# Optimization experiments

Measured on AMD Instinct MI355X. Metric: run time of the kernel, lower is better.

## Reference

```python
import jax, jax.numpy as jnp
import numpy as np

BATCH, SEQ, E, H = 8, 2048, 1024, 1024
LEAK = 0.95
SPECTRAL_RADIUS = 1.2
SPARSITY = 0.1


def setup_inputs() -> dict:
    rng = np.random.default_rng(0)
    x = rng.standard_normal((BATCH, SEQ, E)).astype(np.float32)
    # W_in: kaiming_uniform-like init
    bound = np.sqrt(1.0 / E)
    W_in = rng.uniform(-bound, bound, (H, E)).astype(np.float32)
    # W_res: sparse normal, rescaled to spectral radius 1.2
    W_res = rng.standard_normal((H, H)).astype(np.float32)
    mask = (rng.random((H, H)) > SPARSITY).astype(np.float32)
    W_res *= mask
    rad = np.max(np.abs(np.linalg.eigvals(W_res.astype(np.float64))))
    W_res = (W_res * (SPECTRAL_RADIUS / (rad + 1e-8))).astype(np.float32)
    s = 0.02
    inp = {
        "x": jnp.asarray(x),
        "W_in": jnp.asarray(W_in),
        "W_res": jnp.asarray(W_res),
        "norm_g": jnp.ones((E,), jnp.float32),
        "norm_b": jnp.zeros((E,), jnp.float32),
        "delta_w": jnp.asarray(rng.standard_normal((1, E)).astype(np.float32) * s),
        "delta_b": jnp.zeros((1,), jnp.float32),
        "A": jnp.full((H,), -10.0, jnp.float32),
        "B_w": jnp.asarray(rng.standard_normal((H, E)).astype(np.float32) * s),
        "ro_g": jnp.ones((H,), jnp.float32),
        "ro_b": jnp.zeros((H,), jnp.float32),
        "ro_w": jnp.asarray(rng.standard_normal((E, H)).astype(np.float32) * s),
        "ro_bias": jnp.zeros((E,), jnp.float32),
        "gate_w": jnp.asarray(rng.standard_normal((E, E)).astype(np.float32) * s),
        "gate_b": jnp.zeros((E,), jnp.float32),
    }
    return inp


def _layernorm(x, g, b, eps=1e-5):
    m = jnp.mean(x, axis=-1, keepdims=True)
    v = jnp.mean((x - m) ** 2, axis=-1, keepdims=True)
    return (x - m) * jax.lax.rsqrt(v + eps) * g + b


def reference(x, W_in, W_res, norm_g, norm_b, delta_w, delta_b, A, B_w,
              ro_g, ro_b, ro_w, ro_bias, gate_w, gate_b):
    x_norm = _layernorm(x, norm_g, norm_b)                      # [B,S,E]

    # --- TrueReservoir: leaky tanh RNN (scan over seq) ---
    xin = jnp.einsum('bse,he->bsh', x_norm, W_in)               # [B,S,H]
    h0 = jnp.zeros((x.shape[0], W_res.shape[0]), x.dtype)

    def res_step(h, u):
        new = jnp.tanh(u + h @ W_res.T)
        new = LEAK * new + (1.0 - LEAK) * h
        return new, new

    _, res_states = jax.lax.scan(res_step, h0, jnp.swapaxes(xin, 0, 1))
    res_states = jnp.swapaxes(res_states, 0, 1)                 # [B,S,H]

    ro_in = _layernorm(res_states, ro_g, ro_b)
    reservoir_out = jax.nn.gelu(jnp.einsum('bsh,eh->bse', ro_in, ro_w) + ro_bias,
                                approximate=False)              # [B,S,E]

    # --- selective SSM-style scan ---
    Bx = jnp.einsum('bse,he->bsh', x_norm, B_w)                 # [B,S,H]
    delta = jax.nn.softplus(jnp.einsum('bse,oe->bso', x_norm, delta_w) + delta_b)  # [B,S,1]
    A_bar = jnp.exp(A * delta)                                  # [B,S,H]
    B_bar = Bx * (1.0 - A_bar) / (A + 1e-8)                     # [B,S,H]

    def ssm_step(h, ab):
        a, b = ab
        h = a * h + b
        return h, h

    _, ssm_states = jax.lax.scan(
        ssm_step, h0, (jnp.swapaxes(A_bar, 0, 1), jnp.swapaxes(B_bar, 0, 1)))
    ssm_states = jnp.swapaxes(ssm_states, 0, 1)                 # [B,S,H]

    gate = jax.nn.sigmoid(jnp.einsum('bse,fe->bsf', x, gate_w) + gate_b)  # [B,S,E]
    return reservoir_out * gate + ssm_states * (1.0 - gate)
```

## Files before the change

kernel.cpp:

```cpp
#include <hip/hip_runtime.h>
#include <math.h>

#define B_ 8
#define S_ 2048
#define E_ 1024
#define H_ 1024
#define M_ 16384

typedef __attribute__((ext_vector_type(8))) short short8;
typedef __attribute__((ext_vector_type(4))) float floatx4;

__device__ __forceinline__ void block_reduce2(float &a, float &b) {
#pragma unroll
  for (int off = 32; off > 0; off >>= 1) {
    a += __shfl_down(a, off);
    b += __shfl_down(b, off);
  }
  __shared__ float sa[4], sb[4];
  const int w = threadIdx.x >> 6;
  __syncthreads();
  if ((threadIdx.x & 63) == 0) { sa[w] = a; sb[w] = b; }
  __syncthreads();
  a = sa[0] + sa[1] + sa[2] + sa[3];
  b = sb[0] + sb[1] + sb[2] + sb[3];
}

__device__ __forceinline__ unsigned pack_bf16(float lo, float hi) {
  return __builtin_amdgcn_perm(__float_as_uint(hi) + 0x8000u,
                               __float_as_uint(lo) + 0x8000u, 0x07060302u);
}
__device__ __forceinline__ unsigned pack_hi16(unsigned a, unsigned b) {
  return __builtin_amdgcn_perm(b, a, 0x07060302u);
}

__global__ __launch_bounds__(256) void ln_delta_kernel(
    const float* __restrict__ x, const float* __restrict__ g, const float* __restrict__ bt,
    const float* __restrict__ dw, const float* __restrict__ db,
    unsigned short* __restrict__ xnb, float* __restrict__ delta)
{
  const int row = blockIdx.x;
  const int t = threadIdx.x;
  const float4 v = ((const float4*)(x + (size_t)row * E_))[t];
  float s1 = v.x + v.y + v.z + v.w;
  float s2 = v.x*v.x + v.y*v.y + v.z*v.z + v.w*v.w;
  block_reduce2(s1, s2);
  const float mean = s1 * (1.f / E_);
  const float var  = s2 * (1.f / E_) - mean * mean;
  const float rstd = rsqrtf(var + 1e-5f);
  const float4 g4 = ((const float4*)g)[t];
  const float4 b4 = ((const float4*)bt)[t];
  float4 o;
  o.x = (v.x - mean) * rstd * g4.x + b4.x;
  o.y = (v.y - mean) * rstd * g4.y + b4.y;
  o.z = (v.z - mean) * rstd * g4.z + b4.z;
  o.w = (v.w - mean) * rstd * g4.w + b4.w;
  uint2 p;
  p.x = pack_bf16(o.x, o.y); p.y = pack_bf16(o.z, o.w);
  ((uint2*)(xnb + (size_t)row * E_))[t] = p;
  const float4 d4 = ((const float4*)dw)[t];
  float dd = o.x*d4.x + o.y*d4.y + o.z*d4.z + o.w*d4.w;
  float dummy = 0.f;
  block_reduce2(dd, dummy);
  if (t == 0) {
    const float z = dd + db[0];
    delta[row] = (z > 20.f) ? z : log1pf(__expf(z));
  }
}

__global__ __launch_bounds__(256) void rowstats_kernel(
    const float* __restrict__ res, float2* __restrict__ st)
{
  const int row = blockIdx.x;
  const int t = threadIdx.x;
  const float4 v = ((const float4*)(res + (size_t)row * H_))[t];
  float s1 = v.x + v.y + v.z + v.w;
  float s2 = v.x*v.x + v.y*v.y + v.z*v.z + v.w*v.w;
  block_reduce2(s1, s2);
  if (t == 0) {
    const float m = s1 * (1.f / H_);
    const float var = s2 * (1.f / H_) - m * m;
    st[row] = make_float2(m, rsqrtf(var + 1e-5f));
  }
}

__global__ __launch_bounds__(256) void tobf16_kernel(
    const float* __restrict__ s, unsigned short* __restrict__ d)
{
  const int i = blockIdx.x * 256 + threadIdx.x;
  const float4 v = ((const float4*)s)[i];
  uint2 p;
  p.x = pack_bf16(v.x, v.y); p.y = pack_bf16(v.z, v.w);
  ((uint2*)d)[i] = p;
}

__global__ __launch_bounds__(256) void splitw_kernel(
    const float* __restrict__ s, unsigned short* __restrict__ dh, unsigned short* __restrict__ dl)
{
  const int i = blockIdx.x * 256 + threadIdx.x;
  const float4 v = ((const float4*)s)[i];
  const float sv[4] = {v.x, v.y, v.z, v.w};
  unsigned h[4]; float l[4];
#pragma unroll
  for (int e = 0; e < 4; ++e) {
    h[e] = (__float_as_uint(sv[e]) + 0x8000u) & 0xFFFF0000u;
    l[e] = sv[e] - __uint_as_float(h[e]);
  }
  uint2 ph, pl;
  ph.x = pack_hi16(h[0], h[1]); ph.y = pack_hi16(h[2], h[3]);
  pl.x = pack_bf16(l[0], l[1]); pl.y = pack_bf16(l[2], l[3]);
  ((uint2*)dh)[i] = ph;
  ((uint2*)dl)[i] = pl;
}

__global__ __launch_bounds__(256) void gemm_bb(
    const unsigned short* __restrict__ A, const unsigned short* __restrict__ W,
    float* __restrict__ C)
{
  __shared__ __align__(16) unsigned short As[128 * 40];
  __shared__ __align__(16) unsigned short Ws[128 * 40];
  const int tid  = threadIdx.x;
  const int bn   = blockIdx.x & 7;
  const int bm   = blockIdx.x >> 3;
  const int wave = tid >> 6, lane = tid & 63;
  const int wm = (wave >> 1) * 64, wn = (wave & 1) * 64;
  const int fm = lane & 15, quad = lane >> 4;

  floatx4 acc[4][4];
#pragma unroll
  for (int i = 0; i < 4; ++i)
#pragma unroll
    for (int j = 0; j < 4; ++j) acc[i][j] = (floatx4){0.f, 0.f, 0.f, 0.f};

  const unsigned short* Abase = A + (size_t)bm * 128 * 1024;
  const unsigned short* Wbase = W + (size_t)bn * 128 * 1024;

  for (int k0 = 0; k0 < 1024; k0 += 32) {
    uint2 a2[4], w2[4];
#pragma unroll
    for (int i = 0; i < 4; ++i) {
      const int q = tid + 256 * i;
      const int row = q >> 3, ch = q & 7;
      a2[i] = *(const uint2*)(Abase + (size_t)row * 1024 + k0 + ch * 4);
      w2[i] = *(const uint2*)(Wbase + (size_t)row * 1024 + k0 + ch * 4);
    }
#pragma unroll
    for (int i = 0; i < 4; ++i) {
      const int q = tid + 256 * i;
      const int row = q >> 3, ch = q & 7;
      *(uint2*)(&As[row * 40 + ch * 4]) = a2[i];
      *(uint2*)(&Ws[row * 40 + ch * 4]) = w2[i];
    }
    __syncthreads();
    short8 af[4], wf[4];
#pragma unroll
    for (int i = 0; i < 4; ++i) {
      af[i] = *(const short8*)(&As[(wm + i * 16 + fm) * 40 + quad * 8]);
      wf[i] = *(const short8*)(&Ws[(wn + i * 16 + fm) * 40 + quad * 8]);
    }
#pragma unroll
    for (int i = 0; i < 4; ++i)
#pragma unroll
      for (int j = 0; j < 4; ++j)
        acc[i][j] = __builtin_amdgcn_mfma_f32_16x16x32_bf16(af[i], wf[j], acc[i][j], 0, 0, 0);
    __syncthreads();
  }

#pragma unroll
  for (int i = 0; i < 4; ++i) {
    const int grow0 = bm * 128 + wm + i * 16 + quad * 4;
#pragma unroll
    for (int j = 0; j < 4; ++j) {
      const int gcol = bn * 128 + wn + j * 16 + fm;
#pragma unroll
      for (int r = 0; r < 4; ++r)
        C[(size_t)(grow0 + r) * 1024 + gcol] = acc[i][j][r];
    }
  }
}

template<int ACT>
__global__ __launch_bounds__(256) void gemm_bf16_nt(
    const float* __restrict__ A, const float* __restrict__ W,
    const float* __restrict__ bias, float* __restrict__ C)
{
  __shared__ __align__(16) unsigned short As[128 * 40];
  __shared__ __align__(16) unsigned short Ws[128 * 40];
  const int tid  = threadIdx.x;
  const int bn   = blockIdx.x & 7;
  const int bm   = blockIdx.x >> 3;
  const int wave = tid >> 6, lane = tid & 63;
  const int wm = (wave >> 1) * 64, wn = (wave & 1) * 64;
  const int fm = lane & 15, quad = lane >> 4;

  floatx4 acc[4][4];
#pragma unroll
  for (int i = 0; i < 4; ++i)
#pragma unroll
    for (int j = 0; j < 4; ++j) acc[i][j] = (floatx4){0.f, 0.f, 0.f, 0.f};

  const float* Abase = A + (size_t)bm * 128 * 1024;
  const float* Wbase = W + (size_t)bn * 128 * 1024;

  for (int k0 = 0; k0 < 1024; k0 += 32) {
    float4 a4[4], w4[4];
#pragma unroll
    for (int i = 0; i < 4; ++i) {
      const int q = tid + 256 * i;
      const int row = q >> 3, ch = q & 7;
      a4[i] = *(const float4*)(Abase + (size_t)row * 1024 + k0 + ch * 4);
      w4[i] = *(const float4*)(Wbase + (size_t)row * 1024 + k0 + ch * 4);
    }
#pragma unroll
    for (int i = 0; i < 4; ++i) {
      const int q = tid + 256 * i;
      const int row = q >> 3, ch = q & 7;
      uint2 pa, pw;
      pa.x = pack_bf16(a4[i].x, a4[i].y); pa.y = pack_bf16(a4[i].z, a4[i].w);
      pw.x = pack_bf16(w4[i].x, w4[i].y); pw.y = pack_bf16(w4[i].z, w4[i].w);
      *(uint2*)(&As[row * 40 + ch * 4]) = pa;
      *(uint2*)(&Ws[row * 40 + ch * 4]) = pw;
    }
    __syncthreads();
    short8 af[4], wf[4];
#pragma unroll
    for (int i = 0; i < 4; ++i) {
      af[i] = *(const short8*)(&As[(wm + i * 16 + fm) * 40 + quad * 8]);
      wf[i] = *(const short8*)(&Ws[(wn + i * 16 + fm) * 40 + quad * 8]);
    }
#pragma unroll
    for (int i = 0; i < 4; ++i)
#pragma unroll
      for (int j = 0; j < 4; ++j)
        acc[i][j] = __builtin_amdgcn_mfma_f32_16x16x32_bf16(af[i], wf[j], acc[i][j], 0, 0, 0);
    __syncthreads();
  }

#pragma unroll
  for (int i = 0; i < 4; ++i) {
    const int grow0 = bm * 128 + wm + i * 16 + quad * 4;
#pragma unroll
    for (int j = 0; j < 4; ++j) {
      const int gcol = bn * 128 + wn + j * 16 + fm;
      const float bb = (ACT == 1) ? bias[gcol] : 0.f;
#pragma unroll
      for (int r = 0; r < 4; ++r) {
        float v = acc[i][j][r] + bb;
        if (ACT == 1) v = 1.f / (1.f + __expf(-v));
        C[(size_t)(grow0 + r) * 1024 + gcol] = v;
      }
    }
  }
}

__global__ __launch_bounds__(256) void gemm_readout_mfma(
    const float* __restrict__ A,
    const unsigned short* __restrict__ Wh_g,
    const unsigned short* __restrict__ Wl_g,
    const float* __restrict__ bias,
    const float2* __restrict__ lnst,
    const float* __restrict__ lng, const float* __restrict__ lnb,
    const float* __restrict__ Avec,
    const float* __restrict__ cumd,
    const float* __restrict__ chH,
    const float* __restrict__ gate,
    float* __restrict__ C)
{
  __shared__ __align__(16) unsigned short Ah[128 * 40];
  __shared__ __align__(16) unsigned short Al[128 * 40];
  __shared__ __align__(16) unsigned short Wh[128 * 40];
  __shared__ __align__(16) unsigned short Wl[128 * 40];
  const int tid  = threadIdx.x;
  const int bn   = blockIdx.x & 7;
  const int bm   = blockIdx.x >> 3;
  const int wave = tid >> 6, lane = tid & 63;
  const int wm = (wave >> 1) * 64, wn = (wave & 1) * 64;
  const int fm = lane & 15, quad = lane >> 4;

  floatx4 acc[4][4];
#pragma unroll
  for (int i = 0; i < 4; ++i)
#pragma unroll
    for (int j = 0; j < 4; ++j) acc[i][j] = (floatx4){0.f, 0.f, 0.f, 0.f};

  const float* Abase = A + (size_t)bm * 128 * 1024;
  const unsigned short* Whb = Wh_g + (size_t)bn * 128 * 1024;
  const unsigned short* Wlb = Wl_g + (size_t)bn * 128 * 1024;

  float2 st_i[4];
#pragma unroll
  for (int i = 0; i < 4; ++i) {
    const int q = tid + 256 * i;
    st_i[i] = lnst[bm * 128 + (q >> 3)];
  }

  for (int k0 = 0; k0 < 1024; k0 += 32) {
#pragma unroll
    for (int i = 0; i < 4; ++i) {
      const int q = tid + 256 * i;
      const int row = q >> 3, ch = q & 7;
      float4 a4 = *(const float4*)(Abase + (size_t)row * 1024 + k0 + ch * 4);
      const float4 g4 = *(const float4*)(lng + k0 + ch * 4);
      const float4 b4 = *(const float4*)(lnb + k0 + ch * 4);
      const float2 st = st_i[i];
      a4.x = (a4.x - st.x) * st.y * g4.x + b4.x;
      a4.y = (a4.y - st.x) * st.y * g4.y + b4.y;
      a4.z = (a4.z - st.x) * st.y * g4.z + b4.z;
      a4.w = (a4.w - st.x) * st.y * g4.w + b4.w;
      const float av[4] = {a4.x, a4.y, a4.z, a4.w};
      unsigned ah[4]; float alr[4];
#pragma unroll
      for (int e = 0; e < 4; ++e) {
        ah[e] = (__float_as_uint(av[e]) + 0x8000u) & 0xFFFF0000u;
        alr[e] = av[e] - __uint_as_float(ah[e]);
      }
      uint2 pah, pal;
      pah.x = pack_hi16(ah[0], ah[1]); pah.y = pack_hi16(ah[2], ah[3]);
      pal.x = pack_bf16(alr[0], alr[1]); pal.y = pack_bf16(alr[2], alr[3]);
      *(uint2*)(&Ah[row * 40 + ch * 4]) = pah;
      *(uint2*)(&Al[row * 40 + ch * 4]) = pal;
      *(uint2*)(&Wh[row * 40 + ch * 4]) = *(const uint2*)(Whb + (size_t)row * 1024 + k0 + ch * 4);
      *(uint2*)(&Wl[row * 40 + ch * 4]) = *(const uint2*)(Wlb + (size_t)row * 1024 + k0 + ch * 4);
    }
    __syncthreads();
    short8 afh[4], afl[4], wfh[4], wfl[4];
#pragma unroll
    for (int i = 0; i < 4; ++i) {
      const int ao = (wm + i * 16 + fm) * 40 + quad * 8;
      const int wo = (wn + i * 16 + fm) * 40 + quad * 8;
      afh[i] = *(const short8*)(&Ah[ao]);
      afl[i] = *(const short8*)(&Al[ao]);
      wfh[i] = *(const short8*)(&Wh[wo]);
      wfl[i] = *(const short8*)(&Wl[wo]);
    }
#pragma unroll
    for (int i = 0; i < 4; ++i)
#pragma unroll
      for (int j = 0; j < 4; ++j) {
        acc[i][j] = __builtin_amdgcn_mfma_f32_16x16x32_bf16(afh[i], wfh[j], acc[i][j], 0, 0, 0);
        acc[i][j] = __builtin_amdgcn_mfma_f32_16x16x32_bf16(afl[i], wfh[j], acc[i][j], 0, 0, 0);
        acc[i][j] = __builtin_amdgcn_mfma_f32_16x16x32_bf16(afh[i], wfl[j], acc[i][j], 0, 0, 0);
      }
    __syncthreads();
  }

#pragma unroll
  for (int i = 0; i < 4; ++i) {
    const int grow0 = bm * 128 + wm + i * 16 + quad * 4;
    float cd_r[4];
    int hb_r[4];
#pragma unroll
    for (int r = 0; r < 4; ++r) {
      const int gr = grow0 + r;
      const int b = gr >> 11;
      const int c = (gr & 2047) >> 7;
      cd_r[r] = cumd[gr];
      hb_r[r] = (b * 16 + c) << 10;
    }
#pragma unroll
    for (int j = 0; j < 4; ++j) {
      const int gcol = bn * 128 + wn + j * 16 + fm;
      const float Ae = Avec[gcol];
      const float bb = bias[gcol];
#pragma unroll
      for (int r = 0; r < 4; ++r) {
        const int gr = grow0 + r;
        const size_t off = (size_t)gr * 1024 + gcol;
        const float hin = chH[hb_r[r] + gcol];
        const float lcl = C[off];
        const float gt  = gate[off];
        float v = acc[i][j][r] + bb;
        v = 0.5f * v * (1.f + erff(v * 0.70710678118654752f));
        const float p = __expf(Ae * cd_r[r]);
        const float sst = lcl + p * hin;
        C[off] = v * gt + sst * (1.f - gt);
      }
    }
  }
}

__global__ __launch_bounds__(512, 2) void reservoir_scan_kernel(
    float* __restrict__ xin_res,
    const float* __restrict__ Wres,
    unsigned* __restrict__ hbuf,
    unsigned* __restrict__ unused)
{
  const int tid = threadIdx.x;
  const int wg  = blockIdx.x;
  const int go  = wg >> 4;
  const int mem = wg & 15;
  const int g   = tid >> 6;
  const int l   = tid & 63;
  const int row8 = mem * 64 + g * 8;

  __shared__ __align__(16) float hs[2][1024];

  float4 w4[8][4];
  {
#pragma unroll
    for (int r = 0; r < 8; ++r) {
      const float* wrow = Wres + (size_t)(row8 + r) * 1024 + l * 16;
#pragma unroll
      for (int j = 0; j < 4; ++j) w4[r][j] = *(const float4*)(wrow + 4 * j);
    }
  }

  const int m0 = l & 1, m1 = (l >> 1) & 1, m2 = (l >> 2) & 1;
  const int myrow = row8 + (l & 7);
  float hprev = 0.f;
  const unsigned long long tmask = 0x0000FFFF0000FFFFull;

  const int Pw = (tid >> 1) ^ ((tid >> 6) & 7);
  const int wofs = Pw * 4 + (tid & 1) * 2;

  for (int s = 0; s < S_; ++s) {
    const float u = xin_res[((size_t)go * S_ + s) * H_ + myrow];
    asm volatile("" :: "v"(u));

    const unsigned tag = (unsigned)s & 0xFFFFu;
    const unsigned long long tag2 = (unsigned long long)tag | ((unsigned long long)tag << 32);
    const unsigned long long* hp =
        (const unsigned long long*)(hbuf + (size_t)(s & 1) * 8192 + go * 1024) + tid;
    unsigned long long w;
    for (;;) {
      w = __hip_atomic_load(hp, __ATOMIC_RELAXED, __HIP_MEMORY_SCOPE_AGENT);
      if (((w ^ tag2) & tmask) == 0ull) break;
    }

    float2 hf;
    hf.x = __uint_as_float((unsigned)w & 0xFFFF0000u);
    hf.y = __uint_as_float((unsigned)(w >> 32) & 0xFFFF0000u);
    *(float2*)(&hs[s & 1][wofs]) = hf;
    __syncthreads();

    const float* hbse = hs[s & 1];
    float acc0 = 0.f, acc1 = 0.f, acc2 = 0.f, acc3 = 0.f;
    float acc4 = 0.f, acc5 = 0.f, acc6 = 0.f, acc7 = 0.f;
#pragma unroll
    for (int j = 0; j < 4; ++j) {
      const int P = (4 * l + j) ^ ((l >> 3) & 7);
      const float4 h4 = *(const float4*)(hbse + P * 4);
      acc0 += w4[0][j].x * h4.x + w4[0][j].y * h4.y + w4[0][j].z * h4.z + w4[0][j].w * h4.w;
      acc1 += w4[1][j].x * h4.x + w4[1][j].y * h4.y + w4[1][j].z * h4.z + w4[1][j].w * h4.w;
      acc2 += w4[2][j].x * h4.x + w4[2][j].y * h4.y + w4[2][j].z * h4.z + w4[2][j].w * h4.w;
      acc3 += w4[3][j].x * h4.x + w4[3][j].y * h4.y + w4[3][j].z * h4.z + w4[3][j].w * h4.w;
      acc4 += w4[4][j].x * h4.x + w4[4][j].y * h4.y + w4[4][j].z * h4.z + w4[4][j].w * h4.w;
      acc5 += w4[5][j].x * h4.x + w4[5][j].y * h4.y + w4[5][j].z * h4.z + w4[5][j].w * h4.w;
      acc6 += w4[6][j].x * h4.x + w4[6][j].y * h4.y + w4[6][j].z * h4.z + w4[6][j].w * h4.w;
      acc7 += w4[7][j].x * h4.x + w4[7][j].y * h4.y + w4[7][j].z * h4.z + w4[7][j].w * h4.w;
    }

    float v0 = (m0 ? acc1 : acc0) + __shfl_xor(m0 ? acc0 : acc1, 1);
    float v1 = (m0 ? acc3 : acc2) + __shfl_xor(m0 ? acc2 : acc3, 1);
    float v2 = (m0 ? acc5 : acc4) + __shfl_xor(m0 ? acc4 : acc5, 1);
    float v3 = (m0 ? acc7 : acc6) + __shfl_xor(m0 ? acc6 : acc7, 1);
    float u0 = (m1 ? v1 : v0) + __shfl_xor(m1 ? v0 : v1, 2);
    float u1 = (m1 ? v3 : v2) + __shfl_xor(m1 ? v2 : v3, 2);
    float ps = (m2 ? u1 : u0) + __shfl_xor(m2 ? u0 : u1, 4);
    ps += __shfl_xor(ps, 8);
    ps += __shfl_xor(ps, 16);
    ps += __shfl_xor(ps, 32);

    const float z  = u + ps;
    const float e  = __expf(2.f * z);
    const float hn = 1.f - __fdividef(2.f, e + 1.f);
    const float hv = 0.95f * hn + 0.05f * hprev;
    hprev = hv;

    if (l < 8) {
      const unsigned word = ((__float_as_uint(hv) + 0x8000u) & 0xFFFF0000u)
                          | ((unsigned)(s + 1) & 0xFFFFu);
      __hip_atomic_store(hbuf + (size_t)((s + 1) & 1) * 8192 + go * 1024 + myrow, word,
                         __ATOMIC_RELAXED, __HIP_MEMORY_SCOPE_AGENT);
      xin_res[((size_t)go * S_ + s) * H_ + myrow] = hv;
    }
  }
}

__global__ __launch_bounds__(128) void cumd_kernel(
    const float* __restrict__ delta, float* __restrict__ cumd)
{
  const int t = threadIdx.x;
  const int b = t >> 4, c = t & 15;
  const int base = b * S_ + c * 128;
  float acc = 0.f;
  for (int i = 0; i < 128; ++i) { acc += delta[base + i]; cumd[base + i] = acc; }
}

__global__ __launch_bounds__(256) void ssm_partial_kernel(
    const float* __restrict__ delta, const float* __restrict__ Avec,
    float* __restrict__ bx, float* __restrict__ P)
{
  const int idx = blockIdx.x * 256 + threadIdx.x;
  const int h = idx & 1023;
  const int c = (idx >> 10) & 15;
  const int b = idx >> 14;
  const float Ah = Avec[h];
  const float inv = 1.f / (Ah + 1e-8f);
  const float* dp = delta + b * S_ + c * 128;
  float* xp = bx + ((size_t)(b * S_ + c * 128)) * H_ + h;
  float p = 1.f, hl = 0.f;
  for (int t = 0; t < 128; ++t) {
    const float a = __expf(Ah * dp[t]);
    const float bb = xp[(size_t)t * H_] * (1.f - a) * inv;
    hl = a * hl + bb;
    p *= a;
    xp[(size_t)t * H_] = hl;
  }
  P[(b * 16 + c) * 1024 + h] = p;
}

__global__ __launch_bounds__(256) void ssm_combine_kernel(
    const float* __restrict__ P, const float* __restrict__ local, float* __restrict__ Hin)
{
  const int idx = blockIdx.x * 256 + threadIdx.x;
  const int h = idx & 1023;
  const int b = idx >> 10;
  float hh = 0.f;
#pragma unroll
  for (int c = 0; c < 16; ++c) {
    const int o = (b * 16 + c) * 1024 + h;
    Hin[o] = hh;
    hh = P[o] * hh + local[((size_t)(b * S_ + c * 128 + 127)) * H_ + h];
  }
}

extern "C" void kernel_launch(void* const* d_in, const int* in_sizes, int n_in,
                              void* d_out, int out_size, void* d_ws, size_t ws_size,
                              hipStream_t stream) {
  (void)in_sizes; (void)n_in; (void)out_size; (void)ws_size;
  const float* x      = (const float*)d_in[0];
  const float* W_in   = (const float*)d_in[1];
  const float* W_res  = (const float*)d_in[2];
  const float* norm_g = (const float*)d_in[3];
  const float* norm_b = (const float*)d_in[4];
  const float* dw     = (const float*)d_in[5];
  const float* db     = (const float*)d_in[6];
  const float* Avec   = (const float*)d_in[7];
  const float* B_w    = (const float*)d_in[8];
  const float* ro_g   = (const float*)d_in[9];
  const float* ro_b   = (const float*)d_in[10];
  const float* ro_w   = (const float*)d_in[11];
  const float* ro_bias= (const float*)d_in[12];
  const float* gate_w = (const float*)d_in[13];
  const float* gate_b = (const float*)d_in[14];
  float* out = (float*)d_out;
  float* ws  = (float*)d_ws;

  float*    buf0   = ws;
  float*    buf1   = ws + 16777216;
  float*    delta  = ws + 33554432;
  float*    cumd   = ws + 33570816;
  unsigned* hbuf   = (unsigned*)(ws + 33587200);
  float2*   stats  = (float2*)(ws + 33603712);
  float*    chP    = ws + 33636480;
  float*    chH    = ws + 33767552;
  unsigned short* xnb = (unsigned short*)buf0;
  unsigned short* wib = (unsigned short*)(ws + 33898624);
  unsigned short* bwb = (unsigned short*)(ws + 34422912);
  unsigned short* roh = (unsigned short*)(ws + 34947200);
  unsigned short* rol = (unsigned short*)(ws + 35471488);

  tobf16_kernel<<<1024, 256, 0, stream>>>(W_in, wib);
  tobf16_kernel<<<1024, 256, 0, stream>>>(B_w, bwb);
  splitw_kernel<<<1024, 256, 0, stream>>>(ro_w, roh, rol);
  ln_delta_kernel<<<M_, 256, 0, stream>>>(x, norm_g, norm_b, dw, db, xnb, delta);
  gemm_bb<<<1024, 256, 0, stream>>>(xnb, wib, buf1);
  gemm_bb<<<1024, 256, 0, stream>>>(xnb, bwb, out);
  gemm_bf16_nt<1><<<1024, 256, 0, stream>>>(x, gate_w, gate_b, buf0);
  cumd_kernel<<<1, 128, 0, stream>>>(delta, cumd);
  ssm_partial_kernel<<<512, 256, 0, stream>>>(delta, Avec, out, chP);
  ssm_combine_kernel<<<32, 256, 0, stream>>>(chP, out, chH);
  hipMemsetAsync(hbuf, 0, 2 * 8192 * sizeof(unsigned), stream);
  reservoir_scan_kernel<<<128, 512, 0, stream>>>(buf1, W_res, hbuf, nullptr);
  rowstats_kernel<<<M_, 256, 0, stream>>>(buf1, stats);
  gemm_readout_mfma<<<1024, 256, 0, stream>>>(buf1, roh, rol, ro_bias, stats, ro_g, ro_b,
                                              Avec, cumd, chH, buf0, out);
}
```

Before: 3.989 ms.

## Fuse gate GEMM into reservoir scan launch to overlap on idle CUs

The sigmoid gate GEMM no longer runs as its own kernel. It is folded into the reservoir scan launch as 1024 extra workgroups (block index 128 and up), so the GEMM can fill compute units the 128 latency-bound scan workgroups leave idle. The GEMM blocks use 512 threads but only 256 are active, and shared memory is reused through a common byte buffer. A risk is that GEMM blocks compete with the spin-waiting scan blocks for CU resources and memory bandwidth. The cross-workgroup flag protocol also assumes all 128 scan blocks stay co-resident, which ordering by block index makes likely.

```diff
diff --git a/kernel.cpp b/kernel.cpp
--- a/kernel.cpp
+++ b/kernel.cpp
@@ -178,80 +178,6 @@
   }
 }
 
-template<int ACT>
-__global__ __launch_bounds__(256) void gemm_bf16_nt(
-    const float* __restrict__ A, const float* __restrict__ W,
-    const float* __restrict__ bias, float* __restrict__ C)
-{
-  __shared__ __align__(16) unsigned short As[128 * 40];
-  __shared__ __align__(16) unsigned short Ws[128 * 40];
-  const int tid  = threadIdx.x;
-  const int bn   = blockIdx.x & 7;
-  const int bm   = blockIdx.x >> 3;
-  const int wave = tid >> 6, lane = tid & 63;
-  const int wm = (wave >> 1) * 64, wn = (wave & 1) * 64;
-  const int fm = lane & 15, quad = lane >> 4;
-
-  floatx4 acc[4][4];
-#pragma unroll
-  for (int i = 0; i < 4; ++i)
-#pragma unroll
-    for (int j = 0; j < 4; ++j) acc[i][j] = (floatx4){0.f, 0.f, 0.f, 0.f};
-
-  const float* Abase = A + (size_t)bm * 128 * 1024;
-  const float* Wbase = W + (size_t)bn * 128 * 1024;
-
-  for (int k0 = 0; k0 < 1024; k0 += 32) {
-    float4 a4[4], w4[4];
-#pragma unroll
-    for (int i = 0; i < 4; ++i) {
-      const int q = tid + 256 * i;
-      const int row = q >> 3, ch = q & 7;
-      a4[i] = *(const float4*)(Abase + (size_t)row * 1024 + k0 + ch * 4);
-      w4[i] = *(const float4*)(Wbase + (size_t)row * 1024 + k0 + ch * 4);
-    }
-#pragma unroll
-    for (int i = 0; i < 4; ++i) {
-      const int q = tid + 256 * i;
-      const int row = q >> 3, ch = q & 7;
-      uint2 pa, pw;
-      pa.x = pack_bf16(a4[i].x, a4[i].y); pa.y = pack_bf16(a4[i].z, a4[i].w);
-      pw.x = pack_bf16(w4[i].x, w4[i].y); pw.y = pack_bf16(w4[i].z, w4[i].w);
-      *(uint2*)(&As[row * 40 + ch * 4]) = pa;
-      *(uint2*)(&Ws[row * 40 + ch * 4]) = pw;
-    }
-    __syncthreads();
-    short8 af[4], wf[4];
-#pragma unroll
-    for (int i = 0; i < 4; ++i) {
-      af[i] = *(const short8*)(&As[(wm + i * 16 + fm) * 40 + quad * 8]);
-      wf[i] = *(const short8*)(&Ws[(wn + i * 16 + fm) * 40 + quad * 8]);
-    }
-#pragma unroll
-    for (int i = 0; i < 4; ++i)
-#pragma unroll
-      for (int j = 0; j < 4; ++j)
-        acc[i][j] = __builtin_amdgcn_mfma_f32_16x16x32_bf16(af[i], wf[j], acc[i][j], 0, 0, 0);
-    __syncthreads();
-  }
-
-#pragma unroll
-  for (int i = 0; i < 4; ++i) {
-    const int grow0 = bm * 128 + wm + i * 16 + quad * 4;
-#pragma unroll
-    for (int j = 0; j < 4; ++j) {
-      const int gcol = bn * 128 + wn + j * 16 + fm;
-      const float bb = (ACT == 1) ? bias[gcol] : 0.f;
-#pragma unroll
-      for (int r = 0; r < 4; ++r) {
-        float v = acc[i][j][r] + bb;
-        if (ACT == 1) v = 1.f / (1.f + __expf(-v));
-        C[(size_t)(grow0 + r) * 1024 + gcol] = v;
-      }
-    }
-  }
-}
-
 __global__ __launch_bounds__(256) void gemm_readout_mfma(
     const float* __restrict__ A,
     const unsigned short* __restrict__ Wh_g,
@@ -378,100 +304,179 @@
   }
 }
 
-__global__ __launch_bounds__(512, 2) void reservoir_scan_kernel(
+__global__ __launch_bounds__(512, 2) void scan_gate_kernel(
     float* __restrict__ xin_res,
     const float* __restrict__ Wres,
     unsigned* __restrict__ hbuf,
-    unsigned* __restrict__ unused)
-{
+    const float* __restrict__ x,
+    const float* __restrict__ gate_w,
+    const float* __restrict__ gate_b,
+    float* __restrict__ gateout)
+{
+  __shared__ __align__(16) unsigned char smem[20480];
+  const int wg  = blockIdx.x;
   const int tid = threadIdx.x;
-  const int wg  = blockIdx.x;
-  const int go  = wg >> 4;
-  const int mem = wg & 15;
-  const int g   = tid >> 6;
-  const int l   = tid & 63;
-  const int row8 = mem * 64 + g * 8;
-
-  __shared__ __align__(16) float hs[2][1024];
-
-  float4 w4[8][4];
-  {
+
+  if (wg < 128) {
+    float* hsb = (float*)smem;
+    const int go  = wg >> 4;
+    const int mem = wg & 15;
+    const int g   = tid >> 6;
+    const int l   = tid & 63;
+    const int row8 = mem * 64 + g * 8;
+
+    float4 w4[8][4];
 #pragma unroll
     for (int r = 0; r < 8; ++r) {
       const float* wrow = Wres + (size_t)(row8 + r) * 1024 + l * 16;
 #pragma unroll
       for (int j = 0; j < 4; ++j) w4[r][j] = *(const float4*)(wrow + 4 * j);
     }
-  }
-
-  const int m0 = l & 1, m1 = (l >> 1) & 1, m2 = (l >> 2) & 1;
-  const int myrow = row8 + (l & 7);
-  float hprev = 0.f;
-  const unsigned long long tmask = 0x0000FFFF0000FFFFull;
-
-  const int Pw = (tid >> 1) ^ ((tid >> 6) & 7);
-  const int wofs = Pw * 4 + (tid & 1) * 2;
-
-  for (int s = 0; s < S_; ++s) {
-    const float u = xin_res[((size_t)go * S_ + s) * H_ + myrow];
-    asm volatile("" :: "v"(u));
-
-    const unsigned tag = (unsigned)s & 0xFFFFu;
-    const unsigned long long tag2 = (unsigned long long)tag | ((unsigned long long)tag << 32);
-    const unsigned long long* hp =
-        (const unsigned long long*)(hbuf + (size_t)(s & 1) * 8192 + go * 1024) + tid;
-    unsigned long long w;
-    for (;;) {
-      w = __hip_atomic_load(hp, __ATOMIC_RELAXED, __HIP_MEMORY_SCOPE_AGENT);
-      if (((w ^ tag2) & tmask) == 0ull) break;
-    }
-
-    float2 hf;
-    hf.x = __uint_as_float((unsigned)w & 0xFFFF0000u);
-    hf.y = __uint_as_float((unsigned)(w >> 32) & 0xFFFF0000u);
-    *(float2*)(&hs[s & 1][wofs]) = hf;
-    __syncthreads();
-
-    const float* hbse = hs[s & 1];
-    float acc0 = 0.f, acc1 = 0.f, acc2 = 0.f, acc3 = 0.f;
-    float acc4 = 0.f, acc5 = 0.f, acc6 = 0.f, acc7 = 0.f;
-#pragma unroll
-    for (int j = 0; j < 4; ++j) {
-      const int P = (4 * l + j) ^ ((l >> 3) & 7);
-      const float4 h4 = *(const float4*)(hbse + P * 4);
-      acc0 += w4[0][j].x * h4.x + w4[0][j].y * h4.y + w4[0][j].z * h4.z + w4[0][j].w * h4.w;
-      acc1 += w4[1][j].x * h4.x + w4[1][j].y * h4.y + w4[1][j].z * h4.z + w4[1][j].w * h4.w;
-      acc2 += w4[2][j].x * h4.x + w4[2][j].y * h4.y + w4[2][j].z * h4.z + w4[2][j].w * h4.w;
-      acc3 += w4[3][j].x * h4.x + w4[3][j].y * h4.y + w4[3][j].z * h4.z + w4[3][j].w * h4.w;
-      acc4 += w4[4][j].x * h4.x + w4[4][j].y * h4.y + w4[4][j].z * h4.z + w4[4][j].w * h4.w;
-      acc5 += w4[5][j].x * h4.x + w4[5][j].y * h4.y + w4[5][j].z * h4.z + w4[5][j].w * h4.w;
-      acc6 += w4[6][j].x * h4.x + w4[6][j].y * h4.y + w4[6][j].z * h4.z + w4[6][j].w * h4.w;
-      acc7 += w4[7][j].x * h4.x + w4[7][j].y * h4.y + w4[7][j].z * h4.z + w4[7][j].w * h4.w;
-    }
-
-    float v0 = (m0 ? acc1 : acc0) + __shfl_xor(m0 ? acc0 : acc1, 1);
-    float v1 = (m0 ? acc3 : acc2) + __shfl_xor(m0 ? acc2 : acc3, 1);
-    float v2 = (m0 ? acc5 : acc4) + __shfl_xor(m0 ? acc4 : acc5, 1);
-    float v3 = (m0 ? acc7 : acc6) + __shfl_xor(m0 ? acc6 : acc7, 1);
-    float u0 = (m1 ? v1 : v0) + __shfl_xor(m1 ? v0 : v1, 2);
-    float u1 = (m1 ? v3 : v2) + __shfl_xor(m1 ? v2 : v3, 2);
-    float ps = (m2 ? u1 : u0) + __shfl_xor(m2 ? u0 : u1, 4);
-    ps += __shfl_xor(ps, 8);
-    ps += __shfl_xor(ps, 16);
-    ps += __shfl_xor(ps, 32);
-
-    const float z  = u + ps;
-    const float e  = __expf(2.f * z);
-    const float hn = 1.f - __fdividef(2.f, e + 1.f);
-    const float hv = 0.95f * hn + 0.05f * hprev;
-    hprev = hv;
-
-    if (l < 8) {
-      const unsigned word = ((__float_as_uint(hv) + 0x8000u) & 0xFFFF0000u)
-                          | ((unsigned)(s + 1) & 0xFFFFu);
-      __hip_atomic_store(hbuf + (size_t)((s + 1) & 1) * 8192 + go * 1024 + myrow, word,
-                         __ATOMIC_RELAXED, __HIP_MEMORY_SCOPE_AGENT);
-      xin_res[((size_t)go * S_ + s) * H_ + myrow] = hv;
+
+    const int m0 = l & 1, m1 = (l >> 1) & 1, m2 = (l >> 2) & 1;
+    const int myrow = row8 + (l & 7);
+    float hprev = 0.f;
+    const unsigned long long tmask = 0x0000FFFF0000FFFFull;
+
+    const int Pw = (tid >> 1) ^ ((tid >> 6) & 7);
+    const int wofs = Pw * 4 + (tid & 1) * 2;
+
+    for (int s = 0; s < S_; ++s) {
+      const float u = xin_res[((size_t)go * S_ + s) * H_ + myrow];
+      asm volatile("" :: "v"(u));
+
+      const unsigned tag = (unsigned)s & 0xFFFFu;
+      const unsigned long long tag2 = (unsigned long long)tag | ((unsigned long long)tag << 32);
+      const unsigned long long* hp =
+          (const unsigned long long*)(hbuf + (size_t)(s & 1) * 8192 + go * 1024) + tid;
+      unsigned long long w;
+      for (;;) {
+        w = __hip_atomic_load(hp, __ATOMIC_RELAXED, __HIP_MEMORY_SCOPE_AGENT);
+        if (((w ^ tag2) & tmask) == 0ull) break;
+      }
+
+      float2 hf;
+      hf.x = __uint_as_float((unsigned)w & 0xFFFF0000u);
+      hf.y = __uint_as_float((unsigned)(w >> 32) & 0xFFFF0000u);
+      *(float2*)(hsb + (s & 1) * 1024 + wofs) = hf;
+      __syncthreads();
+
+      const float* hbse = hsb + (s & 1) * 1024;
+      float acc0 = 0.f, acc1 = 0.f, acc2 = 0.f, acc3 = 0.f;
+      float acc4 = 0.f, acc5 = 0.f, acc6 = 0.f, acc7 = 0.f;
+#pragma unroll
+      for (int j = 0; j < 4; ++j) {
+        const int P = (4 * l + j) ^ ((l >> 3) & 7);
+        const float4 h4 = *(const float4*)(hbse + P * 4);
+        acc0 += w4[0][j].x * h4.x + w4[0][j].y * h4.y + w4[0][j].z * h4.z + w4[0][j].w * h4.w;
+        acc1 += w4[1][j].x * h4.x + w4[1][j].y * h4.y + w4[1][j].z * h4.z + w4[1][j].w * h4.w;
+        acc2 += w4[2][j].x * h4.x + w4[2][j].y * h4.y + w4[2][j].z * h4.z + w4[2][j].w * h4.w;
+        acc3 += w4[3][j].x * h4.x + w4[3][j].y * h4.y + w4[3][j].z * h4.z + w4[3][j].w * h4.w;
+        acc4 += w4[4][j].x * h4.x + w4[4][j].y * h4.y + w4[4][j].z * h4.z + w4[4][j].w * h4.w;
+        acc5 += w4[5][j].x * h4.x + w4[5][j].y * h4.y + w4[5][j].z * h4.z + w4[5][j].w * h4.w;
+        acc6 += w4[6][j].x * h4.x + w4[6][j].y * h4.y + w4[6][j].z * h4.z + w4[6][j].w * h4.w;
+        acc7 += w4[7][j].x * h4.x + w4[7][j].y * h4.y + w4[7][j].z * h4.z + w4[7][j].w * h4.w;
+      }
+
+      float v0 = (m0 ? acc1 : acc0) + __shfl_xor(m0 ? acc0 : acc1, 1);
+      float v1 = (m0 ? acc3 : acc2) + __shfl_xor(m0 ? acc2 : acc3, 1);
+      float v2 = (m0 ? acc5 : acc4) + __shfl_xor(m0 ? acc4 : acc5, 1);
+      float v3 = (m0 ? acc7 : acc6) + __shfl_xor(m0 ? acc6 : acc7, 1);
+      float u0 = (m1 ? v1 : v0) + __shfl_xor(m1 ? v0 : v1, 2);
+      float u1 = (m1 ? v3 : v2) + __shfl_xor(m1 ? v2 : v3, 2);
+      float ps = (m2 ? u1 : u0) + __shfl_xor(m2 ? u0 : u1, 4);
+      ps += __shfl_xor(ps, 8);
+      ps += __shfl_xor(ps, 16);
+      ps += __shfl_xor(ps, 32);
+
+      const float z  = u + ps;
+      const float e  = __expf(2.f * z);
+      const float hn = 1.f - __fdividef(2.f, e + 1.f);
+      const float hv = 0.95f * hn + 0.05f * hprev;
+      hprev = hv;
+
+      if (l < 8) {
+        const unsigned word = ((__float_as_uint(hv) + 0x8000u) & 0xFFFF0000u)
+                            | ((unsigned)(s + 1) & 0xFFFFu);
+        __hip_atomic_store(hbuf + (size_t)((s + 1) & 1) * 8192 + go * 1024 + myrow, word,
+                           __ATOMIC_RELAXED, __HIP_MEMORY_SCOPE_AGENT);
+        xin_res[((size_t)go * S_ + s) * H_ + myrow] = hv;
+      }
+    }
+  } else {
+    unsigned short* As = (unsigned short*)smem;
+    unsigned short* Ws = As + 128 * 40;
+    const int bidx = wg - 128;
+    const int bn   = bidx & 7;
+    const int bm   = bidx >> 3;
+    const bool act = tid < 256;
+    const int wave = tid >> 6, lane = tid & 63;
+    const int wm = (wave >> 1) * 64, wn = (wave & 1) * 64;
+    const int fm = lane & 15, quad = lane >> 4;
+
+    floatx4 acc[4][4];
+#pragma unroll
+    for (int i = 0; i < 4; ++i)
+#pragma unroll
+      for (int j = 0; j < 4; ++j) acc[i][j] = (floatx4){0.f, 0.f, 0.f, 0.f};
+
+    const float* Abase = x + (size_t)bm * 128 * 1024;
+    const float* Wbase = gate_w + (size_t)bn * 128 * 1024;
+
+    for (int k0 = 0; k0 < 1024; k0 += 32) {
+      if (act) {
+        float4 a4[4], w4g[4];
+#pragma unroll
+        for (int i = 0; i < 4; ++i) {
+          const int q = tid + 256 * i;
+          const int row = q >> 3, ch = q & 7;
+          a4[i]  = *(const float4*)(Abase + (size_t)row * 1024 + k0 + ch * 4);
+          w4g[i] = *(const float4*)(Wbase + (size_t)row * 1024 + k0 + ch * 4);
+        }
+#pragma unroll
+        for (int i = 0; i < 4; ++i) {
+          const int q = tid + 256 * i;
+          const int row = q >> 3, ch = q & 7;
+          uint2 pa, pw;
+          pa.x = pack_bf16(a4[i].x, a4[i].y);  pa.y = pack_bf16(a4[i].z, a4[i].w);
+          pw.x = pack_bf16(w4g[i].x, w4g[i].y); pw.y = pack_bf16(w4g[i].z, w4g[i].w);
+          *(uint2*)(&As[row * 40 + ch * 4]) = pa;
+          *(uint2*)(&Ws[row * 40 + ch * 4]) = pw;
+        }
+      }
+      __syncthreads();
+      if (act) {
+        short8 af[4], wf[4];
+#pragma unroll
+        for (int i = 0; i < 4; ++i) {
+          af[i] = *(const short8*)(&As[(wm + i * 16 + fm) * 40 + quad * 8]);
+          wf[i] = *(const short8*)(&Ws[(wn + i * 16 + fm) * 40 + quad * 8]);
+        }
+#pragma unroll
+        for (int i = 0; i < 4; ++i)
+#pragma unroll
+          for (int j = 0; j < 4; ++j)
+            acc[i][j] = __builtin_amdgcn_mfma_f32_16x16x32_bf16(af[i], wf[j], acc[i][j], 0, 0, 0);
+      }
+      __syncthreads();
+    }
+
+    if (act) {
+#pragma unroll
+      for (int i = 0; i < 4; ++i) {
+        const int grow0 = bm * 128 + wm + i * 16 + quad * 4;
+#pragma unroll
+        for (int j = 0; j < 4; ++j) {
+          const int gcol = bn * 128 + wn + j * 16 + fm;
+          const float bb = gate_b[gcol];
+#pragma unroll
+          for (int r = 0; r < 4; ++r) {
+            float v = acc[i][j][r] + bb;
+            v = 1.f / (1.f + __expf(-v));
+            gateout[(size_t)(grow0 + r) * 1024 + gcol] = v;
+          }
+        }
+      }
     }
   }
 }
@@ -566,12 +571,11 @@
   ln_delta_kernel<<<M_, 256, 0, stream>>>(x, norm_g, norm_b, dw, db, xnb, delta);
   gemm_bb<<<1024, 256, 0, stream>>>(xnb, wib, buf1);
   gemm_bb<<<1024, 256, 0, stream>>>(xnb, bwb, out);
-  gemm_bf16_nt<1><<<1024, 256, 0, stream>>>(x, gate_w, gate_b, buf0);
   cumd_kernel<<<1, 128, 0, stream>>>(delta, cumd);
   ssm_partial_kernel<<<512, 256, 0, stream>>>(delta, Avec, out, chP);
   ssm_combine_kernel<<<32, 256, 0, stream>>>(chP, out, chH);
   hipMemsetAsync(hbuf, 0, 2 * 8192 * sizeof(unsigned), stream);
-  reservoir_scan_kernel<<<128, 512, 0, stream>>>(buf1, W_res, hbuf, nullptr);
+  scan_gate_kernel<<<1152, 512, 0, stream>>>(buf1, W_res, hbuf, x, gate_w, gate_b, buf0);
   rowstats_kernel<<<M_, 256, 0, stream>>>(buf1, stats);
   gemm_readout_mfma<<<1024, 256, 0, stream>>>(buf1, roh, rol, ro_bias, stats, ro_g, ro_b,
                                               Avec, cumd, chH, buf0, out);
```

After: 3.848 ms. -3.5%, faster.
